# Kernel tuning notes

Measured on AMD Instinct MI355X. Metric: run time of the kernel, lower is better.

## Reference

```python
import jax, jax.numpy as jnp
import numpy as np

CHANNELS = 512
GROUPS = 32
EPS = 1e-6


def setup_inputs() -> dict:
    key = jax.random.key(0)
    ks = jax.random.split(key, 10)
    C = CHANNELS
    s = 1.0 / np.sqrt(C)
    return {
        "hidden_states": jax.random.normal(ks[0], (4, 64, 64, C), dtype=jnp.float32),
        "gn_scale": jnp.ones((C,), dtype=jnp.float32),
        "gn_bias": jnp.zeros((C,), dtype=jnp.float32),
        "wq": jax.random.normal(ks[1], (C, C), dtype=jnp.float32) * s,
        "bq": jnp.zeros((C,), dtype=jnp.float32),
        "wk": jax.random.normal(ks[2], (C, C), dtype=jnp.float32) * s,
        "bk": jnp.zeros((C,), dtype=jnp.float32),
        "wv": jax.random.normal(ks[3], (C, C), dtype=jnp.float32) * s,
        "bv": jnp.zeros((C,), dtype=jnp.float32),
        "wo": jax.random.normal(ks[4], (C, C), dtype=jnp.float32) * s,
        "bo": jnp.zeros((C,), dtype=jnp.float32),
    }


def reference(hidden_states, gn_scale, gn_bias, wq, bq, wk, bk, wv, bv, wo, bo):
    B, H, W, C = hidden_states.shape
    residual = hidden_states
    L = H * W
    x = hidden_states.reshape(B, L, C)

    # GroupNorm: stats over (spatial, channels-within-group), per batch per group
    xg = x.reshape(B, L, GROUPS, C // GROUPS)
    mean = jnp.mean(xg, axis=(1, 3), keepdims=True)
    var = jnp.var(xg, axis=(1, 3), keepdims=True)
    xn = ((xg - mean) * jax.lax.rsqrt(var + EPS)).reshape(B, L, C)
    xn = xn * gn_scale + gn_bias

    # QKV projections (heads=1, head_dim=C)
    q = xn @ wq + bq
    k = xn @ wk + bk
    v = xn @ wv + bv

    scale = 1.0 / jnp.sqrt(jnp.asarray(C, dtype=q.dtype))
    scores = jnp.einsum('bld,bsd->bls', q, k) * scale  # [B, L, L]
    attn = jax.nn.softmax(scores, axis=-1)
    out = jnp.einsum('bls,bsd->bld', attn, v)

    out = out @ wo + bo
    return out.reshape(B, H, W, C) + residual
```

## Files before the change

kernel.cpp:

```cpp
#include <hip/hip_runtime.h>
#include <hip/hip_bf16.h>
#include <stdint.h>

#define BATCH 4
#define SEQ   4096
#define CH    512
#define NGRP  32
#define GEPS  1e-6f

typedef short  short8  __attribute__((ext_vector_type(8)));
typedef float  floatx4 __attribute__((ext_vector_type(4)));
typedef long   longx2  __attribute__((ext_vector_type(2)));

static __device__ __forceinline__ short bf16b(float f) {
    __hip_bfloat16 h = __float2bfloat16(f);
    return __builtin_bit_cast(short, h);
}
static __device__ __forceinline__ float bf2f(short s) {
    unsigned u = ((unsigned)(unsigned short)s) << 16;
    return __builtin_bit_cast(float, u);
}
static __device__ __forceinline__ char fp8b(float f) {
    int pk = __builtin_amdgcn_cvt_pk_fp8_f32(f, f, 0, false);
    return (char)(pk & 0xff);
}

static __device__ __forceinline__ void dma16(const void* g, void* l) {
    __builtin_amdgcn_global_load_lds(
        (const __attribute__((address_space(1))) unsigned int*)g,
        (__attribute__((address_space(3))) unsigned int*)l, 16, 0, 0);
}

static __device__ __forceinline__ float rowmax16(float x) {
    int xi = __builtin_bit_cast(int, x);
    x = fmaxf(x, __builtin_bit_cast(float, __builtin_amdgcn_update_dpp(xi, xi, 0x128, 0xf, 0xf, true)));
    xi = __builtin_bit_cast(int, x);
    x = fmaxf(x, __builtin_bit_cast(float, __builtin_amdgcn_update_dpp(xi, xi, 0x124, 0xf, 0xf, true)));
    xi = __builtin_bit_cast(int, x);
    x = fmaxf(x, __builtin_bit_cast(float, __builtin_amdgcn_update_dpp(xi, xi, 0x122, 0xf, 0xf, true)));
    xi = __builtin_bit_cast(int, x);
    x = fmaxf(x, __builtin_bit_cast(float, __builtin_amdgcn_update_dpp(xi, xi, 0x121, 0xf, 0xf, true)));
    return x;
}

__global__ __launch_bounds__(256) void gn_partial_kernel(const float* __restrict__ x,
                                                         float* __restrict__ statsraw) {
    int blk = blockIdx.x;
    int t = threadIdx.x;
    size_t row0 = (size_t)blk * 64;
    int qd = t & 127;
    int rh = t >> 7;
    const float* base = x + row0 * 512 + qd * 4;
    float s1 = 0.f, s2 = 0.f;
    #pragma unroll 4
    for (int i = 0; i < 32; ++i) {
        int r = rh + i * 2;
        float4 v = *reinterpret_cast<const float4*>(base + (size_t)r * 512);
        s1 += v.x + v.y + v.z + v.w;
        s2 += v.x * v.x + v.y * v.y + v.z * v.z + v.w * v.w;
    }
    __shared__ float a1[256], a2[256];
    a1[t] = s1; a2[t] = s2;
    __syncthreads();
    if (t < 32) {
        float u1 = 0.f, u2 = 0.f;
        #pragma unroll
        for (int e = 0; e < 4; ++e) {
            u1 += a1[t * 4 + e] + a1[128 + t * 4 + e];
            u2 += a2[t * 4 + e] + a2[128 + t * 4 + e];
        }
        int b = (int)(row0 >> 12);
        atomicAdd(&statsraw[(b * 32 + t) * 2],     u1);
        atomicAdd(&statsraw[(b * 32 + t) * 2 + 1], u2);
    }
}

__global__ __launch_bounds__(256) void gn_apply_kernel(const float* __restrict__ x,
                                                       const float* __restrict__ statsraw,
                                                       const float* __restrict__ gsc,
                                                       const float* __restrict__ gbs,
                                                       short* __restrict__ xn) {
    int i4 = blockIdx.x * 256 + threadIdx.x;
    int base = i4 * 4;
    int b = base >> 21;
    int c = base & 511;
    int sidx = (b * 32 + (c >> 4)) * 2;
    float s1 = statsraw[sidx], s2 = statsraw[sidx + 1];
    float mean = s1 * (1.f / 65536.f);
    float var  = s2 * (1.f / 65536.f) - mean * mean;
    float rstd = rsqrtf(var + GEPS);
    float4 xv = reinterpret_cast<const float4*>(x)[i4];
    float4 sv = *reinterpret_cast<const float4*>(gsc + c);
    float4 bv = *reinterpret_cast<const float4*>(gbs + c);
    union { short s[4]; uint2 u; } p;
    p.s[0] = bf16b((xv.x - mean) * rstd * sv.x + bv.x);
    p.s[1] = bf16b((xv.y - mean) * rstd * sv.y + bv.y);
    p.s[2] = bf16b((xv.z - mean) * rstd * sv.z + bv.z);
    p.s[3] = bf16b((xv.w - mean) * rstd * sv.w + bv.w);
    reinterpret_cast<uint2*>(xn)[i4] = p.u;
}

__global__ __launch_bounds__(256) void wtrans_kernel(const float* __restrict__ w0,
                                                     const float* __restrict__ w1,
                                                     const float* __restrict__ w2,
                                                     const float* __restrict__ w3,
                                                     short* __restrict__ wT) {
    const float* w = (blockIdx.z == 0) ? w0 : (blockIdx.z == 1) ? w1
                   : (blockIdx.z == 2) ? w2 : w3;
    short* out = wT + (size_t)blockIdx.z * CH * CH;
    int n0 = blockIdx.x * 32, k0 = blockIdx.y * 32;
    int tx = threadIdx.x, ty = threadIdx.y;
    __shared__ float s[32][33];
    #pragma unroll
    for (int i = 0; i < 4; ++i) {
        int kk = ty + i * 8;
        s[kk][tx] = w[(size_t)(k0 + kk) * CH + n0 + tx];
    }
    __syncthreads();
    #pragma unroll
    for (int i = 0; i < 4; ++i) {
        int nn = ty + i * 8;
        out[(size_t)(n0 + nn) * CH + k0 + tx] = bf16b(s[tx][nn]);
    }
}

__global__ __launch_bounds__(256) void gemm_qkv_kernel(const short* __restrict__ A,
                                                       const short* __restrict__ wT,
                                                       const float* __restrict__ bq,
                                                       const float* __restrict__ bk,
                                                       const float* __restrict__ bv,
                                                       char* __restrict__ q8,
                                                       char* __restrict__ k8,
                                                       char* __restrict__ vT8) {
    __shared__ short As[128 * 64];
    __shared__ short Bs[128 * 64];
    __shared__ char  vls[128 * 144];
    int m0 = blockIdx.x * 128;
    int nblk = blockIdx.y;
    int which = nblk >> 2;
    int n0 = (nblk & 3) * 128;
    const short* BT = wT + (size_t)which * 512 * 512;
    const float* bias = (which == 0) ? bq : (which == 1) ? bk : bv;
    int t = threadIdx.x;
    int w = t >> 6, lane = t & 63;
    int wr = w >> 1, wc = w & 1;
    int l15 = lane & 15, l4 = lane >> 4;
    floatx4 acc[4][4];
    #pragma unroll
    for (int i = 0; i < 4; ++i)
        #pragma unroll
        for (int j = 0; j < 4; ++j) acc[i][j] = (floatx4){0.f, 0.f, 0.f, 0.f};

    for (int k0 = 0; k0 < 512; k0 += 64) {
        __syncthreads();
        #pragma unroll
        for (int i = 0; i < 4; ++i) {
            int c = i * 256 + t;
            int row = c >> 3, j = (c & 7) ^ (row & 7);
            dma16(&A[(size_t)(m0 + row) * 512 + k0 + j * 8], &As[(c & ~63) * 8]);
            dma16(&BT[(size_t)(n0 + row) * 512 + k0 + j * 8], &Bs[(c & ~63) * 8]);
        }
        __syncthreads();
        #pragma unroll
        for (int kk = 0; kk < 64; kk += 32) {
            short8 af[4], bf[4];
            #pragma unroll
            for (int i = 0; i < 4; ++i) {
                int row = wr * 64 + i * 16 + l15;
                int j = (kk >> 3) + l4;
                af[i] = *reinterpret_cast<const short8*>(&As[(row * 8 + (j ^ (l15 & 7))) * 8]);
            }
            #pragma unroll
            for (int j2 = 0; j2 < 4; ++j2) {
                int row = wc * 64 + j2 * 16 + l15;
                int j = (kk >> 3) + l4;
                bf[j2] = *reinterpret_cast<const short8*>(&Bs[(row * 8 + (j ^ (l15 & 7))) * 8]);
            }
            #pragma unroll
            for (int i = 0; i < 4; ++i)
                #pragma unroll
                for (int j2 = 0; j2 < 4; ++j2)
                    acc[i][j2] = __builtin_amdgcn_mfma_f32_16x16x32_bf16(af[i], bf[j2], acc[i][j2], 0, 0, 0);
        }
    }
    if (which == 0) {
        #pragma unroll
        for (int i = 0; i < 4; ++i)
            #pragma unroll
            for (int j = 0; j < 4; ++j)
                #pragma unroll
                for (int r = 0; r < 4; ++r) {
                    int row = m0 + wr * 64 + i * 16 + l4 * 4 + r;
                    int col = n0 + wc * 64 + j * 16 + l15;
                    q8[(size_t)row * 512 + col] = fp8b(acc[i][j][r] + bias[col]);
                }
    } else if (which == 1) {
        #pragma unroll
        for (int i = 0; i < 4; ++i)
            #pragma unroll
            for (int j = 0; j < 4; ++j)
                #pragma unroll
                for (int r = 0; r < 4; ++r) {
                    int row = m0 + wr * 64 + i * 16 + l4 * 4 + r;
                    int col = n0 + wc * 64 + j * 16 + l15;
                    int bb = row >> 12, s = row & 4095;
                    size_t idx = (size_t)bb * 2097152 + (size_t)(s >> 5) * 16384
                               + (s & 15) * 1024 + ((s >> 4) & 1) * 8
                               + (col >> 3) * 16 + (col & 7);
                    k8[idx] = fp8b(acc[i][j][r] + bias[col]);
                }
    } else {
        __syncthreads();
        #pragma unroll
        for (int i = 0; i < 4; ++i)
            #pragma unroll
            for (int j = 0; j < 4; ++j)
                #pragma unroll
                for (int r = 0; r < 4; ++r) {
                    int rl = wr * 64 + i * 16 + l4 * 4 + r;
                    int rp = (rl & ~31) | (((rl & 15) << 1) | ((rl >> 4) & 1));
                    int cl = wc * 64 + j * 16 + l15;
                    vls[cl * 144 + rp] = fp8b(acc[i][j][r] + bias[n0 + cl]);
                }
        __syncthreads();
        int b = m0 >> 12, l0 = m0 & 4095;
        #pragma unroll
        for (int p = 0; p < 4; ++p) {
            int slot = p * 256 + t;
            int c = slot >> 3, off = (slot & 7) * 16;
            uint4 v;
            __builtin_memcpy(&v, &vls[c * 144 + off], 16);
            int dcol = n0 + c;
            int g = dcol >> 5, rr = dcol & 15, h = (dcol >> 4) & 1;
            int s = l0 + off;
            int sb = s >> 5, mb = (s & 31) >> 3;
            char* dst = vT8 + (size_t)b * 2097152 + (size_t)sb * 16384
                      + (size_t)((((g * 16 + rr) * 4 + mb) * 16) + h * 8);
            unsigned long long lo = ((unsigned long long)v.y << 32) | v.x;
            unsigned long long hi = ((unsigned long long)v.w << 32) | v.z;
            *reinterpret_cast<unsigned long long*>(dst)      = lo;
            *reinterpret_cast<unsigned long long*>(dst + 16) = hi;
        }
    }
}

__global__ __launch_bounds__(256) void gemm_bt_kernel(const short* __restrict__ Opart,
                                                      const float* __restrict__ ml,
                                                      const short* __restrict__ BT,
                                                      const float* __restrict__ bias,
                                                      float* __restrict__ outf,
                                                      const float* __restrict__ resid) {
    __shared__ short As[128 * 64];
    __shared__ short Bs[128 * 64];
    int m0 = blockIdx.x * 128, n0 = blockIdx.y * 128;
    int t = threadIdx.x;
    int w = t >> 6, lane = t & 63;
    int wr = w >> 1, wc = w & 1;
    int l15 = lane & 15, l4 = lane >> 4;
    const size_t PART = (size_t)BATCH * SEQ;
    floatx4 acc[4][4];
    #pragma unroll
    for (int i = 0; i < 4; ++i)
        #pragma unroll
        for (int j = 0; j < 4; ++j) acc[i][j] = (floatx4){0.f, 0.f, 0.f, 0.f};

    for (int k0 = 0; k0 < 512; k0 += 64) {
        __syncthreads();
        #pragma unroll
        for (int i = 0; i < 4; ++i) {
            int c = i * 256 + t;
            int rl = c >> 3, j = (c & 7) ^ (rl & 7);
            size_t rowg = (size_t)(m0 + rl);
            const short* s0 = Opart + rowg * 512 + k0 + j * 8;
            const short* s1 = s0 + PART * 512;
            uint4 a0 = *reinterpret_cast<const uint4*>(s0);
            uint4 a1 = *reinterpret_cast<const uint4*>(s1);
            float mA = ml[rowg * 2],          lA = ml[rowg * 2 + 1];
            float mB = ml[(PART + rowg) * 2], lB = ml[(PART + rowg) * 2 + 1];
            float mm = fmaxf(mA, mB);
            float e0 = exp2f(mA - mm), e1 = exp2f(mB - mm);
            float inv = 1.f / (e0 * lA + e1 * lB);
            e0 *= inv; e1 *= inv;
            union { uint4 u; short s[8]; } ua, ub, uo;
            ua.u = a0; ub.u = a1;
            #pragma unroll
            for (int e = 0; e < 8; ++e)
                uo.s[e] = bf16b(bf2f(ua.s[e]) * e0 + bf2f(ub.s[e]) * e1);
            *reinterpret_cast<uint4*>(&As[c * 8]) = uo.u;
            dma16(&BT[(size_t)(n0 + rl) * 512 + k0 + j * 8], &Bs[(c & ~63) * 8]);
        }
        __syncthreads();
        #pragma unroll
        for (int kk = 0; kk < 64; kk += 32) {
            short8 af[4], bf[4];
            #pragma unroll
            for (int i = 0; i < 4; ++i) {
                int row = wr * 64 + i * 16 + l15;
                int j = (kk >> 3) + l4;
                af[i] = *reinterpret_cast<const short8*>(&As[(row * 8 + (j ^ (l15 & 7))) * 8]);
            }
            #pragma unroll
            for (int j2 = 0; j2 < 4; ++j2) {
                int row = wc * 64 + j2 * 16 + l15;
                int j = (kk >> 3) + l4;
                bf[j2] = *reinterpret_cast<const short8*>(&Bs[(row * 8 + (j ^ (l15 & 7))) * 8]);
            }
            #pragma unroll
            for (int i = 0; i < 4; ++i)
                #pragma unroll
                for (int j2 = 0; j2 < 4; ++j2)
                    acc[i][j2] = __builtin_amdgcn_mfma_f32_16x16x32_bf16(af[i], bf[j2], acc[i][j2], 0, 0, 0);
        }
    }
    #pragma unroll
    for (int i = 0; i < 4; ++i)
        #pragma unroll
        for (int j = 0; j < 4; ++j)
            #pragma unroll
            for (int r = 0; r < 4; ++r) {
                int row = m0 + wr * 64 + i * 16 + l4 * 4 + r;
                int col = n0 + wc * 64 + j * 16 + l15;
                float vv = acc[i][j][r] + bias[col];
                outf[(size_t)row * 512 + col] = vv + resid[(size_t)row * 512 + col];
            }
}

__global__ __launch_bounds__(512, 1) void flash_kernel(const char* __restrict__ q8,
                                                       const char* __restrict__ k8,
                                                       const char* __restrict__ v8,
                                                       short* __restrict__ Opart,
                                                       float* __restrict__ ml) {
    __shared__ __align__(16) char smem[70656];
    int bx = blockIdx.x;
    int pb = bx & 7;
    int part = pb >> 2, b = pb & 3;
    int q0 = (bx >> 3) * 128;
    int t = threadIdx.x, w = t >> 6, lane = t & 63;
    int l15 = lane & 15, l4 = lane >> 4;
    const float c2 = 0.06375873735f;
    const float MARGIN = 7.2134752f;

    long qf[16];
    {
        const char* qrow = q8 + ((size_t)b * SEQ + q0 + w * 16 + l15) * 512;
        #pragma unroll
        for (int ks = 0; ks < 16; ++ks)
            qf[ks] = *reinterpret_cast<const long*>(qrow + ks * 32 + l4 * 8);
    }

    floatx4 acc[32];
    #pragma unroll
    for (int i = 0; i < 32; ++i) acc[i] = (floatx4){0.f, 0.f, 0.f, 0.f};
    floatx4 lacc = (floatx4){0.f, 0.f, 0.f, 0.f};
    float mused[4] = {-1e30f, -1e30f, -1e30f, -1e30f};

    const long ones = 0x3838383838383838L;

    const char* kbase = k8 + (size_t)b * SEQ * 512;
    const char* vbase = v8 + (size_t)b * 512 * SEQ;
    const int sb0 = part * 64;

    const int ksw = l15 & 7;
    const int vsw = (l15 >> 1) & 3;
    const char* kA_E = smem + ((l15 * 64 + (l4 ^ ksw)) << 4);
    const char* kA_O = smem + ((l15 * 64 + ((4 + l4) ^ ksw)) << 4);
    const char* vA   = smem + 32768 + ((l15 * 4 + (l4 ^ vsw)) << 4);
    char* Ps = smem + 65536 + w * 640;

    int kSrc[2], vSrc[2];
    #pragma unroll
    for (int i = 0; i < 2; ++i) {
        int c = i * 512 + t;
        kSrc[i] = (((c & ~63) | ((c & 63) ^ ((c >> 6) & 7))) << 4);
        vSrc[i] = (((c & ~3)  | ((c & 3)  ^ ((c >> 3) & 3))) << 4);
    }
    const int ldsD = (t & ~63) << 4;

    auto stage = [&](int sb, int buf) {
        const char* kt = kbase + (size_t)sb * 16384;
        const char* vt = vbase + (size_t)sb * 16384;
        char* Kd = smem + buf * 16384 + ldsD;
        char* Vd = smem + 32768 + buf * 16384 + ldsD;
        #pragma unroll
        for (int i = 0; i < 2; ++i) dma16(kt + kSrc[i], Kd + i * 8192);
        #pragma unroll
        for (int i = 0; i < 2; ++i) dma16(vt + vSrc[i], Vd + i * 8192);
    };

    stage(sb0, 0);
    __syncthreads();

    for (int it = 0; it < 64; ++it) {
        int cur = it & 1;
        int coff = cur << 14;
        if (it + 1 < 64) stage(sb0 + it + 1, 1 - cur);

        floatx4 sa0 = (floatx4){0.f, 0.f, 0.f, 0.f};
        floatx4 sa1 = (floatx4){0.f, 0.f, 0.f, 0.f};
        #pragma unroll
        for (int j = 0; j < 8; ++j) {
            longx2 kE = *reinterpret_cast<const longx2*>(kA_E + coff + j * 128);
            longx2 kO = *reinterpret_cast<const longx2*>(kA_O + coff + j * 128);
            sa0 = __builtin_amdgcn_mfma_f32_16x16x32_fp8_fp8(qf[2 * j],     kE[0], sa0, 0, 0, 0);
            sa1 = __builtin_amdgcn_mfma_f32_16x16x32_fp8_fp8(qf[2 * j],     kE[1], sa1, 0, 0, 0);
            sa0 = __builtin_amdgcn_mfma_f32_16x16x32_fp8_fp8(qf[2 * j + 1], kO[0], sa0, 0, 0, 0);
            sa1 = __builtin_amdgcn_mfma_f32_16x16x32_fp8_fp8(qf[2 * j + 1], kO[1], sa1, 0, 0, 0);
        }

        float v0[4], v1[4], nm4[4];
        bool need = false;
        #pragma unroll
        for (int r = 0; r < 4; ++r) {
            v0[r] = sa0[r] * c2; v1[r] = sa1[r] * c2;
            nm4[r] = rowmax16(fmaxf(v0[r], v1[r]));
            need |= (nm4[r] > mused[r] + MARGIN);
        }
        if (__ballot(need)) {
            #pragma unroll
            for (int r = 0; r < 4; ++r) {
                float nm = fmaxf(mused[r], nm4[r]);
                float al = exp2f(mused[r] - nm);
                lacc[r] *= al;
                #pragma unroll
                for (int i = 0; i < 32; ++i) acc[i][r] *= al;
                mused[r] = nm;
            }
        }
        #pragma unroll
        for (int r = 0; r < 4; ++r) {
            int pk = __builtin_amdgcn_cvt_pk_fp8_f32(exp2f(v0[r] - mused[r]),
                                                     exp2f(v1[r] - mused[r]), 0, false);
            *reinterpret_cast<short*>(Ps + (l4 * 4 + r) * 40 + l15 * 2) = (short)pk;
        }

        long pf;
        __builtin_memcpy(&pf, (const char*)__builtin_assume_aligned(Ps + l15 * 40 + l4 * 8, 8), 8);
        lacc = __builtin_amdgcn_mfma_f32_16x16x32_fp8_fp8(pf, ones, lacc, 0, 0, 0);
        #pragma unroll
        for (int g = 0; g < 16; ++g) {
            longx2 vv = *reinterpret_cast<const longx2*>(vA + coff + g * 1024);
            acc[2 * g]     = __builtin_amdgcn_mfma_f32_16x16x32_fp8_fp8(pf, vv[0], acc[2 * g],     0, 0, 0);
            acc[2 * g + 1] = __builtin_amdgcn_mfma_f32_16x16x32_fp8_fp8(pf, vv[1], acc[2 * g + 1], 0, 0, 0);
        }

        __syncthreads();
    }

    short* obase = Opart + (((size_t)part * BATCH + b) * SEQ + q0 + w * 16) * 512;
    #pragma unroll
    for (int r = 0; r < 4; ++r) {
        #pragma unroll
        for (int tt = 0; tt < 32; ++tt)
            obase[(size_t)(l4 * 4 + r) * 512 + tt * 16 + l15] = bf16b(acc[tt][r]);
    }
    if (l15 == 0) {
        #pragma unroll
        for (int r = 0; r < 4; ++r) {
            size_t rowg = ((size_t)part * BATCH + b) * SEQ + q0 + w * 16 + l4 * 4 + r;
            ml[rowg * 2]     = mused[r];
            ml[rowg * 2 + 1] = lacc[r];
        }
    }
}

extern "C" void kernel_launch(void* const* d_in, const int* in_sizes, int n_in,
                              void* d_out, int out_size, void* d_ws, size_t ws_size,
                              hipStream_t stream) {
    const float* x   = (const float*)d_in[0];
    const float* gsc = (const float*)d_in[1];
    const float* gbs = (const float*)d_in[2];
    const float* wq  = (const float*)d_in[3];
    const float* bq  = (const float*)d_in[4];
    const float* wk  = (const float*)d_in[5];
    const float* bk  = (const float*)d_in[6];
    const float* wv  = (const float*)d_in[7];
    const float* bv  = (const float*)d_in[8];
    const float* wo  = (const float*)d_in[9];
    const float* bo  = (const float*)d_in[10];
    float* out = (float*)d_out;

    char* ws = (char*)d_ws;
    const size_t MB = 1ull << 20;
    short* xn    = (short*)ws;
    char*  q8    = (char*)(ws + 16 * MB);
    char*  k8    = (char*)(ws + 24 * MB);
    char*  vT8   = (char*)(ws + 32 * MB);
    short* Opart = (short*)(ws + 40 * MB);
    short* wT    = (short*)(ws + 72 * MB);
    float* stats = (float*)(ws + 74 * MB);
    float* ml    = (float*)(ws + 74 * MB + 65536);

    hipMemsetAsync(stats, 0, 256 * sizeof(float), stream);
    gn_partial_kernel<<<256, 256, 0, stream>>>(x, stats);
    gn_apply_kernel<<<8192, 256, 0, stream>>>(x, stats, gsc, gbs, xn);
    wtrans_kernel<<<dim3(16, 16, 4), dim3(32, 8), 0, stream>>>(wq, wk, wv, wo, wT);

    short* woT = wT + 786432;

    gemm_qkv_kernel<<<dim3(128, 12), 256, 0, stream>>>(xn, wT, bq, bk, bv, q8, k8, vT8);
    flash_kernel<<<256, 512, 0, stream>>>(q8, k8, vT8, Opart, ml);
    gemm_bt_kernel<<<dim3(128, 4), 256, 0, stream>>>(Opart, ml, woT, bo, out, x);
}
```

Measured before the change: 292.6 us.

## Stage Q and K epilogue stores through LDS and merge GN stats with weight transpose

The Q and K epilogues of the QKV GEMM now write fp8 results into shared memory first, with an XOR swizzle for K. They then emit 16-byte vectorized global stores instead of scattered single-byte stores. Separately, the GroupNorm partial-stats kernel and the weight-transpose kernel are merged into one launch to remove a kernel launch and let both run concurrently. The cost is an extra LDS round trip and barrier in the epilogue, plus a more complex combined kernel.

```diff
diff --git a/kernel.cpp b/kernel.cpp
--- a/kernel.cpp
+++ b/kernel.cpp
@@ -43,35 +43,61 @@
     return x;
 }
 
-__global__ __launch_bounds__(256) void gn_partial_kernel(const float* __restrict__ x,
-                                                         float* __restrict__ statsraw) {
+__global__ __launch_bounds__(256) void gn_wt_kernel(const float* __restrict__ x,
+                                                    float* __restrict__ statsraw,
+                                                    const float* __restrict__ w0,
+                                                    const float* __restrict__ w1,
+                                                    const float* __restrict__ w2,
+                                                    const float* __restrict__ w3,
+                                                    short* __restrict__ wT) {
+    __shared__ float a1[256], a2[256];
+    __shared__ float trs[32][33];
     int blk = blockIdx.x;
     int t = threadIdx.x;
-    size_t row0 = (size_t)blk * 64;
-    int qd = t & 127;
-    int rh = t >> 7;
-    const float* base = x + row0 * 512 + qd * 4;
-    float s1 = 0.f, s2 = 0.f;
-    #pragma unroll 4
-    for (int i = 0; i < 32; ++i) {
-        int r = rh + i * 2;
-        float4 v = *reinterpret_cast<const float4*>(base + (size_t)r * 512);
-        s1 += v.x + v.y + v.z + v.w;
-        s2 += v.x * v.x + v.y * v.y + v.z * v.z + v.w * v.w;
-    }
-    __shared__ float a1[256], a2[256];
-    a1[t] = s1; a2[t] = s2;
-    __syncthreads();
-    if (t < 32) {
-        float u1 = 0.f, u2 = 0.f;
-        #pragma unroll
-        for (int e = 0; e < 4; ++e) {
-            u1 += a1[t * 4 + e] + a1[128 + t * 4 + e];
-            u2 += a2[t * 4 + e] + a2[128 + t * 4 + e];
-        }
-        int b = (int)(row0 >> 12);
-        atomicAdd(&statsraw[(b * 32 + t) * 2],     u1);
-        atomicAdd(&statsraw[(b * 32 + t) * 2 + 1], u2);
+    if (blk < 256) {
+        size_t row0 = (size_t)blk * 64;
+        int qd = t & 127;
+        int rh = t >> 7;
+        const float* base = x + row0 * 512 + qd * 4;
+        float s1 = 0.f, s2 = 0.f;
+        #pragma unroll 4
+        for (int i = 0; i < 32; ++i) {
+            int r = rh + i * 2;
+            float4 v = *reinterpret_cast<const float4*>(base + (size_t)r * 512);
+            s1 += v.x + v.y + v.z + v.w;
+            s2 += v.x * v.x + v.y * v.y + v.z * v.z + v.w * v.w;
+        }
+        a1[t] = s1; a2[t] = s2;
+        __syncthreads();
+        if (t < 32) {
+            float u1 = 0.f, u2 = 0.f;
+            #pragma unroll
+            for (int e = 0; e < 4; ++e) {
+                u1 += a1[t * 4 + e] + a1[128 + t * 4 + e];
+                u2 += a2[t * 4 + e] + a2[128 + t * 4 + e];
+            }
+            int b = (int)(row0 >> 12);
+            atomicAdd(&statsraw[(b * 32 + t) * 2],     u1);
+            atomicAdd(&statsraw[(b * 32 + t) * 2 + 1], u2);
+        }
+    } else {
+        int bz = (blk - 256) >> 8;
+        int rem = (blk - 256) & 255;
+        int n0 = (rem & 15) * 32, k0 = (rem >> 4) * 32;
+        const float* w = (bz == 0) ? w0 : (bz == 1) ? w1 : (bz == 2) ? w2 : w3;
+        short* out = wT + (size_t)bz * CH * CH;
+        int tx = t & 31, ty = t >> 5;
+        #pragma unroll
+        for (int i = 0; i < 4; ++i) {
+            int kk = ty + i * 8;
+            trs[kk][tx] = w[(size_t)(k0 + kk) * CH + n0 + tx];
+        }
+        __syncthreads();
+        #pragma unroll
+        for (int i = 0; i < 4; ++i) {
+            int nn = ty + i * 8;
+            out[(size_t)(n0 + nn) * CH + k0 + tx] = bf16b(trs[tx][nn]);
+        }
     }
 }
 
@@ -98,30 +124,6 @@
     p.s[2] = bf16b((xv.z - mean) * rstd * sv.z + bv.z);
     p.s[3] = bf16b((xv.w - mean) * rstd * sv.w + bv.w);
     reinterpret_cast<uint2*>(xn)[i4] = p.u;
-}
-
-__global__ __launch_bounds__(256) void wtrans_kernel(const float* __restrict__ w0,
-                                                     const float* __restrict__ w1,
-                                                     const float* __restrict__ w2,
-                                                     const float* __restrict__ w3,
-                                                     short* __restrict__ wT) {
-    const float* w = (blockIdx.z == 0) ? w0 : (blockIdx.z == 1) ? w1
-                   : (blockIdx.z == 2) ? w2 : w3;
-    short* out = wT + (size_t)blockIdx.z * CH * CH;
-    int n0 = blockIdx.x * 32, k0 = blockIdx.y * 32;
-    int tx = threadIdx.x, ty = threadIdx.y;
-    __shared__ float s[32][33];
-    #pragma unroll
-    for (int i = 0; i < 4; ++i) {
-        int kk = ty + i * 8;
-        s[kk][tx] = w[(size_t)(k0 + kk) * CH + n0 + tx];
-    }
-    __syncthreads();
-    #pragma unroll
-    for (int i = 0; i < 4; ++i) {
-        int nn = ty + i * 8;
-        out[(size_t)(n0 + nn) * CH + k0 + tx] = bf16b(s[tx][nn]);
-    }
 }
 
 __global__ __launch_bounds__(256) void gemm_qkv_kernel(const short* __restrict__ A,
@@ -190,10 +192,19 @@
             for (int j = 0; j < 4; ++j)
                 #pragma unroll
                 for (int r = 0; r < 4; ++r) {
-                    int row = m0 + wr * 64 + i * 16 + l4 * 4 + r;
-                    int col = n0 + wc * 64 + j * 16 + l15;
-                    q8[(size_t)row * 512 + col] = fp8b(acc[i][j][r] + bias[col]);
+                    int rl = wr * 64 + i * 16 + l4 * 4 + r;
+                    int cl = wc * 64 + j * 16 + l15;
+                    vls[rl * 144 + cl] = fp8b(acc[i][j][r] + bias[n0 + cl]);
                 }
+        __syncthreads();
+        #pragma unroll
+        for (int p = 0; p < 4; ++p) {
+            int slot = p * 256 + t;
+            int c = slot >> 3, off = (slot & 7) * 16;
+            uint4 v;
+            __builtin_memcpy(&v, &vls[c * 144 + off], 16);
+            *reinterpret_cast<uint4*>(&q8[(size_t)(m0 + c) * 512 + n0 + off]) = v;
+        }
     } else if (which == 1) {
         #pragma unroll
         for (int i = 0; i < 4; ++i)
@@ -201,14 +212,25 @@
             for (int j = 0; j < 4; ++j)
                 #pragma unroll
                 for (int r = 0; r < 4; ++r) {
-                    int row = m0 + wr * 64 + i * 16 + l4 * 4 + r;
-                    int col = n0 + wc * 64 + j * 16 + l15;
-                    int bb = row >> 12, s = row & 4095;
-                    size_t idx = (size_t)bb * 2097152 + (size_t)(s >> 5) * 16384
-                               + (s & 15) * 1024 + ((s >> 4) & 1) * 8
-                               + (col >> 3) * 16 + (col & 7);
-                    k8[idx] = fp8b(acc[i][j][r] + bias[col]);
+                    int rl = wr * 64 + i * 16 + l4 * 4 + r;
+                    int cl = wc * 64 + j * 16 + l15;
+                    int sblk = rl >> 5, srow = rl & 15, hp = (rl >> 4) & 1;
+                    int ch = (cl >> 3) ^ (srow & 7);
+                    vls[sblk * 4096 + srow * 256 + ch * 16 + hp * 8 + (cl & 7)]
+                        = fp8b(acc[i][j][r] + bias[n0 + cl]);
                 }
+        __syncthreads();
+        int bb = m0 >> 12, sb0 = (m0 & 4095) >> 5;
+        #pragma unroll
+        for (int p = 0; p < 4; ++p) {
+            int u = p * 256 + t;
+            int sblk = u >> 8, srow = (u >> 4) & 15, ch = u & 15;
+            uint4 v;
+            __builtin_memcpy(&v, &vls[sblk * 4096 + srow * 256 + ((ch ^ (srow & 7)) * 16)], 16);
+            char* dst = k8 + (size_t)bb * 2097152 + (size_t)(sb0 + sblk) * 16384
+                      + srow * 1024 + n0 * 2 + ch * 16;
+            *reinterpret_cast<uint4*>(dst) = v;
+        }
     } else {
         __syncthreads();
         #pragma unroll
@@ -491,9 +513,8 @@
     float* ml    = (float*)(ws + 74 * MB + 65536);
 
     hipMemsetAsync(stats, 0, 256 * sizeof(float), stream);
-    gn_partial_kernel<<<256, 256, 0, stream>>>(x, stats);
+    gn_wt_kernel<<<1280, 256, 0, stream>>>(x, stats, wq, wk, wv, wo, wT);
     gn_apply_kernel<<<8192, 256, 0, stream>>>(x, stats, gsc, gbs, xn);
-    wtrans_kernel<<<dim3(16, 16, 4), dim3(32, 8), 0, stream>>>(wq, wk, wv, wo, wT);
 
     short* woT = wT + 786432;
 
```

New measurement: 288.8 us. About the same (-1.3%).
